# Performance work log

Measured on AMD Instinct MI355X. Metric: run time of the kernel, lower is better.

Reference implementation:

```python
import jax, jax.numpy as jnp
import numpy as np

B, X, C = 8, 256, 256  # batch, feature axis, topfreq

def setup_inputs() -> dict:
    key = jax.random.key(0)
    k1, k2, k3, k4 = jax.random.split(key, 4)
    return {
        "amplitude": jax.random.normal(k1, (B, X, C), dtype=jnp.float32),
        "phase": jax.random.normal(k2, (B, X, C), dtype=jnp.float32),
        "A": jax.random.normal(k3, (C, C), dtype=jnp.float32),
        "w_amplitude": jnp.asarray(0.5, dtype=jnp.float32),
        "w_phase": jnp.asarray(0.5, dtype=jnp.float32),
        # uniform noise for gumbel sampling; keep away from 0 to avoid -log(-log(0))
        "gumbel_u": jax.random.uniform(k4, (B, C, C, 2), dtype=jnp.float32, minval=1e-6, maxval=1.0),
    }

def reference(amplitude, phase, A, w_amplitude, w_phase, gumbel_u):
    # pairwise diffs: (b, x, c, c)
    a_diff = amplitude[..., :, None] - amplitude[..., None, :]
    p_diff = phase[..., :, None] - phase[..., None, :]
    fused = w_amplitude * a_diff + w_phase * p_diff
    # einsum 'dd,bxcd->bxcd' == multiply by diag(A) along last dim
    temp = jnp.diagonal(A) * fused
    # einsum 'bxcd,bxcd->bcd' == sum of squares over x
    dist = jnp.sum(temp * temp, axis=1)  # (b, c, c)
    exp_dist = 1.0 / (dist + 1e-10)
    eye = jnp.eye(C, dtype=exp_dist.dtype)
    off_diag = 1.0 - eye
    exp_dist = exp_dist * off_diag
    exp_max = jax.lax.stop_gradient(jnp.max(exp_dist, axis=-1, keepdims=True))
    p = exp_dist / exp_max
    p = (p * off_diag + eye) * 0.99  # (b, c, c) in (0, 0.99]
    # bernoulli via 2-class gumbel-softmax (tau=1, hard, straight-through)
    logit = jnp.log(p / (1.0 - p))
    logits = jnp.stack([logit, -logit], axis=-1)  # (b, c, c, 2)
    g = -jnp.log(-jnp.log(gumbel_u))
    y = jax.nn.softmax(logits + g, axis=-1)
    y0 = y[..., 0]
    hard0 = (y0 > y[..., 1]).astype(y.dtype)
    sample = hard0 - jax.lax.stop_gradient(y0) + y0  # straight-through
    mask = sample.mean(axis=0)  # (c, c)
    return mask
```

## Files before the change

### kernel.cpp

```cpp
#include <hip/hip_runtime.h>

#define BB 8
#define XX 256
#define CC 256
#define TCD 8
#define TCE 4
#define G  8
#define SPLIT 4
#define XH (XX / SPLIT)



__device__ __forceinline__ void epilogue(
    float dist0, float dist1, float dist2, float dist3,
    int b, int c0, int d, const float* __restrict__ gu,
    float* __restrict__ out, float (*wmax)[4])
{
    float ed[TCE];
    ed[0] = (d == c0)     ? 0.0f : __fdiv_rn(1.0f, __fadd_rn(dist0, 1e-10f));
    ed[1] = (d == c0 + 1) ? 0.0f : __fdiv_rn(1.0f, __fadd_rn(dist1, 1e-10f));
    ed[2] = (d == c0 + 2) ? 0.0f : __fdiv_rn(1.0f, __fadd_rn(dist2, 1e-10f));
    ed[3] = (d == c0 + 3) ? 0.0f : __fdiv_rn(1.0f, __fadd_rn(dist3, 1e-10f));

    const int wave = threadIdx.x >> 6;
    const int lane = threadIdx.x & 63;
#pragma unroll
    for (int j = 0; j < TCE; ++j) {
        float v = ed[j];
#pragma unroll
        for (int m = 1; m < 64; m <<= 1) v = fmaxf(v, __shfl_xor(v, m));
        if (lane == 0) wmax[j][wave] = v;
    }
    __syncthreads();

#pragma unroll
    for (int j = 0; j < TCE; ++j) {
        const int c = c0 + j;
        float em = fmaxf(fmaxf(wmax[j][0], wmax[j][1]), fmaxf(wmax[j][2], wmax[j][3]));
        float p;
        if (d == c) {
            p = 0.99f;
        } else {
            p = __fmul_rn(__fdiv_rn(ed[j], em), 0.99f);
        }
        float logit = logf(__fdiv_rn(p, __fsub_rn(1.0f, p)));

        const float2 g2 = *(const float2*)(gu + (((size_t)b * CC + c) * CC + d) * 2);
        float g0 = -logf(-logf(g2.x));
        float g1 = -logf(-logf(g2.y));

        float a0 = __fadd_rn(logit, g0);
        float a1 = __fadd_rn(-logit, g1);
        float m  = fmaxf(a0, a1);
        float e0 = expf(__fsub_rn(a0, m));
        float e1 = expf(__fsub_rn(a1, m));
        float s  = __fadd_rn(e0, e1);
        float y0 = __fdiv_rn(e0, s);
        float y1 = __fdiv_rn(e1, s);
        if (y0 > y1) {
            atomicAdd(&out[(size_t)c * CC + d], 0.125f);
        }
    }
}


__global__ __launch_bounds__(256) void k_u(
    const float* __restrict__ amp, const float* __restrict__ ph,
    const float* __restrict__ wAp, const float* __restrict__ wPp,
    float* __restrict__ u, float* __restrict__ out)
{
    const float wa = wAp[0], wp = wPp[0];
    const int i = blockIdx.x * 256 + threadIdx.x;
    const float4 a = ((const float4*)amp)[i];
    const float4 p = ((const float4*)ph)[i];
    float4 r;
    r.x = __fadd_rn(__fmul_rn(wa, a.x), __fmul_rn(wp, p.x));
    r.y = __fadd_rn(__fmul_rn(wa, a.y), __fmul_rn(wp, p.y));
    r.z = __fadd_rn(__fmul_rn(wa, a.z), __fmul_rn(wp, p.z));
    r.w = __fadd_rn(__fmul_rn(wa, a.w), __fmul_rn(wp, p.w));
    ((float4*)u)[i] = r;

    if (blockIdx.x < 64) {
        ((float4*)out)[blockIdx.x * 256 + threadIdx.x] = make_float4(0.f, 0.f, 0.f, 0.f);
    }
}

#define ULOAD(BU, GIDX) {                                  \
    const float* _p = ud_ptr + (size_t)(GIDX) * G * CC;    \
    _Pragma("unroll")                                      \
    for (int i = 0; i < G; ++i) BU[i] = _p[(size_t)i * CC]; }

#define UCOMP(BU, GIDX) {                                  \
    const int _xb = (GIDX) * G;                            \
    _Pragma("unroll")                                      \
    for (int i = 0; i < G; ++i) {                          \
        const float udv = BU[i];                           \
        const float4 cA = colsU[_xb + i][0];               \
        const float4 cB = colsU[_xb + i][1];               \
        gacc0 = fmaf(cA.x, udv, gacc0);                    \
        gacc1 = fmaf(cA.y, udv, gacc1);                    \
        gacc2 = fmaf(cA.z, udv, gacc2);                    \
        gacc3 = fmaf(cA.w, udv, gacc3);                    \
        gacc4 = fmaf(cB.x, udv, gacc4);                    \
        gacc5 = fmaf(cB.y, udv, gacc5);                    \
        gacc6 = fmaf(cB.z, udv, gacc6);                    \
        gacc7 = fmaf(cB.w, udv, gacc7);                    \
        sacc  = fmaf(udv, udv, sacc);                      \
    } }

__global__ __launch_bounds__(256, 4) void k_dist(
    const float* __restrict__ u,
    float* __restrict__ wsd)
{
    const int d    = threadIdx.x;
    const int c0   = blockIdx.x * TCD;
    const int b    = blockIdx.y;
    const int x0   = blockIdx.z * XH;

    __shared__ float4 colsU[XH][2];
    if (threadIdx.x < 2 * XH) {
        const int x = threadIdx.x >> 1;
        const int h = threadIdx.x & 1;
        colsU[x][h] =
            *(const float4*)(u + ((size_t)b * XX + x0 + x) * CC + c0 + 4 * h);
    }
    __syncthreads();

    const float* ud_ptr = u + ((size_t)b * XX + x0) * CC + d;

    float gacc0 = 0.f, gacc1 = 0.f, gacc2 = 0.f, gacc3 = 0.f;
    float gacc4 = 0.f, gacc5 = 0.f, gacc6 = 0.f, gacc7 = 0.f, sacc = 0.f;

    constexpr int NGH = XH / G;
    float b0[G], b1[G];
    ULOAD(b0, 0)
    for (int g = 0; g + 2 < NGH; g += 2) {
        ULOAD(b1, g + 1)
        UCOMP(b0, g)
        ULOAD(b0, g + 2)
        UCOMP(b1, g + 1)
    }
    ULOAD(b1, NGH - 1)
    UCOMP(b0, NGH - 2)
    UCOMP(b1, NGH - 1)

    __shared__ float sS[CC];
    sS[d] = sacc;
    __syncthreads();

    float* w = wsd + (((size_t)blockIdx.z * BB + b) * CC + c0) * CC + d;
    w[0 * CC] = fmaf(-2.0f, gacc0, __fadd_rn(sS[c0 + 0], sacc));
    w[1 * CC] = fmaf(-2.0f, gacc1, __fadd_rn(sS[c0 + 1], sacc));
    w[2 * CC] = fmaf(-2.0f, gacc2, __fadd_rn(sS[c0 + 2], sacc));
    w[3 * CC] = fmaf(-2.0f, gacc3, __fadd_rn(sS[c0 + 3], sacc));
    w[4 * CC] = fmaf(-2.0f, gacc4, __fadd_rn(sS[c0 + 4], sacc));
    w[5 * CC] = fmaf(-2.0f, gacc5, __fadd_rn(sS[c0 + 5], sacc));
    w[6 * CC] = fmaf(-2.0f, gacc6, __fadd_rn(sS[c0 + 6], sacc));
    w[7 * CC] = fmaf(-2.0f, gacc7, __fadd_rn(sS[c0 + 7], sacc));
}

__global__ __launch_bounds__(256, 4) void k_epi(
    const float* __restrict__ wsd, const float* __restrict__ A,
    const float* __restrict__ gu,  float* __restrict__ out)
{
    const int d  = threadIdx.x;
    const int c0 = blockIdx.x * TCE;
    const int b  = blockIdx.y;

    const float dAd  = A[(size_t)d * CC + d];
    const float dAd2 = __fmul_rn(dAd, dAd);

    float dist[TCE];
#pragma unroll
    for (int j = 0; j < TCE; ++j) {
        const size_t ro = ((size_t)b * CC + c0 + j) * CC + d;
        float p = wsd[ro];
#pragma unroll
        for (int h = 1; h < SPLIT; ++h)
            p = __fadd_rn(p, wsd[(size_t)h * BB * CC * CC + ro]);
        dist[j] = __fmul_rn(dAd2, p);
    }

    __shared__ float wmax[TCE][4];
    epilogue(dist[0], dist[1], dist[2], dist[3], b, c0, d, gu, out, wmax);
}


#define STEPU(UC, ACC) {                         \
    float diff = __fsub_rn(UC, ud);              \
    float t    = __fmul_rn(dAd, diff);           \
    float sq   = __fmul_rn(t, t);                \
    ACC = __fadd_rn(ACC, sq);                    \
}

#define LOADG(BA, BP, GIDX) {                    \
    const float* _a = ampbd + (size_t)(GIDX) * G * CC; \
    const float* _p = phbd  + (size_t)(GIDX) * G * CC; \
    _Pragma("unroll")                            \
    for (int i = 0; i < G; ++i) {                \
        BA[i] = _a[(size_t)i * CC];              \
        BP[i] = _p[(size_t)i * CC];              \
    }                                            \
}

#define COMPG(BA, BP, GIDX) {                    \
    const int _xb = (GIDX) * G;                  \
    _Pragma("unroll")                            \
    for (int i = 0; i < G; ++i) {                \
        const float av = BA[i];                  \
        const float pv = BP[i];                  \
        const float ud = __fadd_rn(__fmul_rn(wa, av), __fmul_rn(wp, pv)); \
        const float4 uc = cols[_xb + i];         \
        STEPU(uc.x, acc0)                        \
        STEPU(uc.y, acc1)                        \
        STEPU(uc.z, acc2)                        \
        STEPU(uc.w, acc3)                        \
    }                                            \
}

__global__ __launch_bounds__(256, 2) void k_fused(
    const float* __restrict__ amp, const float* __restrict__ ph,
    const float* __restrict__ A,   const float* __restrict__ wAp,
    const float* __restrict__ wPp, const float* __restrict__ gu,
    float* __restrict__ out)
{
    const int d  = threadIdx.x;
    const int c0 = blockIdx.x * TCE;
    const int b  = blockIdx.y;

    const float wa = wAp[0];
    const float wp = wPp[0];

    __shared__ float4 cols[XX];
    {
        const int x = threadIdx.x;
        const size_t base = ((size_t)b * XX + x) * CC + c0;
        const float4 a4 = *(const float4*)(amp + base);
        const float4 p4 = *(const float4*)(ph  + base);
        float4 uu;
        uu.x = __fadd_rn(__fmul_rn(wa, a4.x), __fmul_rn(wp, p4.x));
        uu.y = __fadd_rn(__fmul_rn(wa, a4.y), __fmul_rn(wp, p4.y));
        uu.z = __fadd_rn(__fmul_rn(wa, a4.z), __fmul_rn(wp, p4.z));
        uu.w = __fadd_rn(__fmul_rn(wa, a4.w), __fmul_rn(wp, p4.w));
        cols[x] = uu;
    }
    __syncthreads();

    const float dAd = A[(size_t)d * CC + d];
    const float* ampbd = amp + (size_t)b * XX * CC + d;
    const float* phbd  = ph  + (size_t)b * XX * CC + d;

    float acc0 = 0.0f, acc1 = 0.0f, acc2 = 0.0f, acc3 = 0.0f;
    constexpr int NG = XX / G;
    {
        float b0A[G], b0P[G], b1A[G], b1P[G];
        LOADG(b0A, b0P, 0)
        for (int g = 0; g + 2 < NG; g += 2) {
            LOADG(b1A, b1P, g + 1)
            COMPG(b0A, b0P, g)
            LOADG(b0A, b0P, g + 2)
            COMPG(b1A, b1P, g + 1)
        }
        LOADG(b1A, b1P, NG - 1)
        COMPG(b0A, b0P, NG - 2)
        COMPG(b1A, b1P, NG - 1)
    }

    __shared__ float wmax[TCE][4];
    epilogue(acc0, acc1, acc2, acc3, b, c0, d, gu, out, wmax);
}

extern "C" void kernel_launch(void* const* d_in, const int* in_sizes, int n_in,
                              void* d_out, int out_size, void* d_ws, size_t ws_size,
                              hipStream_t stream) {
    const float* amp = (const float*)d_in[0];
    const float* ph  = (const float*)d_in[1];
    const float* A   = (const float*)d_in[2];
    const float* wa  = (const float*)d_in[3];
    const float* wp  = (const float*)d_in[4];
    const float* gu  = (const float*)d_in[5];
    float* out = (float*)d_out;

    const size_t uElems = (size_t)BB * XX * CC;
    const size_t pElems = (size_t)SPLIT * BB * CC * CC;
    const size_t need = (uElems + pElems) * sizeof(float);
    if (ws_size >= need) {
        float* ud  = (float*)d_ws;
        float* wsd = ud + uElems;
        k_u<<<uElems / 4 / 256, 256, 0, stream>>>(amp, ph, wa, wp, ud, out);
        dim3 g1(CC / TCD, BB, SPLIT);
        k_dist<<<g1, 256, 0, stream>>>(ud, wsd);
        dim3 g2(CC / TCE, BB);
        k_epi<<<g2, 256, 0, stream>>>(wsd, A, gu, out);
    } else {
        hipMemsetAsync(out, 0, (size_t)CC * CC * sizeof(float), stream);
        dim3 g(CC / TCE, BB);
        k_fused<<<g, 256, 0, stream>>>(amp, ph, A, wa, wp, gu, out);
    }
}
```

Before: 83.42 us.

## Fuse split-X distance and epilogue kernels into one 1024-thread block

Merges the split-X distance kernel and the epilogue kernel into a single kernel with 1024 threads per block, where four thread groups each handle a quarter of the X axis and reduce their partials through shared memory instead of a global workspace. This removes one kernel launch and the round trip of 4*B*C*C partial sums through global memory. In exchange the grid shrinks to 256 blocks of 1024 threads, each block needing about 45 KB of shared memory, which may limit occupancy and per-CU parallelism.

```diff
diff --git a/kernel.cpp b/kernel.cpp
--- a/kernel.cpp
+++ b/kernel.cpp
@@ -6,62 +6,9 @@
 #define TCD 8
 #define TCE 4
 #define G  8
-#define SPLIT 4
-#define XH (XX / SPLIT)
-
-
-
-__device__ __forceinline__ void epilogue(
-    float dist0, float dist1, float dist2, float dist3,
-    int b, int c0, int d, const float* __restrict__ gu,
-    float* __restrict__ out, float (*wmax)[4])
-{
-    float ed[TCE];
-    ed[0] = (d == c0)     ? 0.0f : __fdiv_rn(1.0f, __fadd_rn(dist0, 1e-10f));
-    ed[1] = (d == c0 + 1) ? 0.0f : __fdiv_rn(1.0f, __fadd_rn(dist1, 1e-10f));
-    ed[2] = (d == c0 + 2) ? 0.0f : __fdiv_rn(1.0f, __fadd_rn(dist2, 1e-10f));
-    ed[3] = (d == c0 + 3) ? 0.0f : __fdiv_rn(1.0f, __fadd_rn(dist3, 1e-10f));
-
-    const int wave = threadIdx.x >> 6;
-    const int lane = threadIdx.x & 63;
-#pragma unroll
-    for (int j = 0; j < TCE; ++j) {
-        float v = ed[j];
-#pragma unroll
-        for (int m = 1; m < 64; m <<= 1) v = fmaxf(v, __shfl_xor(v, m));
-        if (lane == 0) wmax[j][wave] = v;
-    }
-    __syncthreads();
-
-#pragma unroll
-    for (int j = 0; j < TCE; ++j) {
-        const int c = c0 + j;
-        float em = fmaxf(fmaxf(wmax[j][0], wmax[j][1]), fmaxf(wmax[j][2], wmax[j][3]));
-        float p;
-        if (d == c) {
-            p = 0.99f;
-        } else {
-            p = __fmul_rn(__fdiv_rn(ed[j], em), 0.99f);
-        }
-        float logit = logf(__fdiv_rn(p, __fsub_rn(1.0f, p)));
-
-        const float2 g2 = *(const float2*)(gu + (((size_t)b * CC + c) * CC + d) * 2);
-        float g0 = -logf(-logf(g2.x));
-        float g1 = -logf(-logf(g2.y));
-
-        float a0 = __fadd_rn(logit, g0);
-        float a1 = __fadd_rn(-logit, g1);
-        float m  = fmaxf(a0, a1);
-        float e0 = expf(__fsub_rn(a0, m));
-        float e1 = expf(__fsub_rn(a1, m));
-        float s  = __fadd_rn(e0, e1);
-        float y0 = __fdiv_rn(e0, s);
-        float y1 = __fdiv_rn(e1, s);
-        if (y0 > y1) {
-            atomicAdd(&out[(size_t)c * CC + d], 0.125f);
-        }
-    }
-}
+#define NCH 4
+#define XH (XX / NCH)
+
 
 
 __global__ __launch_bounds__(256) void k_u(
@@ -91,7 +38,7 @@
     for (int i = 0; i < G; ++i) BU[i] = _p[(size_t)i * CC]; }
 
 #define UCOMP(BU, GIDX) {                                  \
-    const int _xb = (GIDX) * G;                            \
+    const int _xb = x0 + (GIDX) * G;                       \
     _Pragma("unroll")                                      \
     for (int i = 0; i < G; ++i) {                          \
         const float udv = BU[i];                           \
@@ -108,83 +55,176 @@
         sacc  = fmaf(udv, udv, sacc);                      \
     } }
 
-__global__ __launch_bounds__(256, 4) void k_dist(
+__global__ __launch_bounds__(1024, 4) void k_main(
     const float* __restrict__ u,
-    float* __restrict__ wsd)
+    const float* __restrict__ A,
+    const float* __restrict__ gu,
+    float* __restrict__ out)
 {
-    const int d    = threadIdx.x;
-    const int c0   = blockIdx.x * TCD;
-    const int b    = blockIdx.y;
-    const int x0   = blockIdx.z * XH;
-
-    __shared__ float4 colsU[XH][2];
-    if (threadIdx.x < 2 * XH) {
-        const int x = threadIdx.x >> 1;
-        const int h = threadIdx.x & 1;
-        colsU[x][h] =
-            *(const float4*)(u + ((size_t)b * XX + x0 + x) * CC + c0 + 4 * h);
-    }
-    __syncthreads();
+    const int tid = threadIdx.x;
+    const int c0  = blockIdx.x * TCD;
+    const int b   = blockIdx.y;
+
+    __shared__ float4 colsU[XX][2];
+    __shared__ float  sS[NCH][CC];
+    __shared__ float  pw[NCH][CC][9];
+    __shared__ float  wmax[TCD][4];
+
+    if (tid < 512) {
+        const int x = tid >> 1, h = tid & 1;
+        colsU[x][h] = *(const float4*)(u + ((size_t)b * XX + x) * CC + c0 + 4 * h);
+    }
+    __syncthreads();
+
+    const int d     = tid & 255;
+    const int chunk = tid >> 8;
+    const int x0    = chunk * XH;
 
     const float* ud_ptr = u + ((size_t)b * XX + x0) * CC + d;
 
-    float gacc0 = 0.f, gacc1 = 0.f, gacc2 = 0.f, gacc3 = 0.f;
-    float gacc4 = 0.f, gacc5 = 0.f, gacc6 = 0.f, gacc7 = 0.f, sacc = 0.f;
+    float gacc0=0.f, gacc1=0.f, gacc2=0.f, gacc3=0.f;
+    float gacc4=0.f, gacc5=0.f, gacc6=0.f, gacc7=0.f, sacc=0.f;
 
     constexpr int NGH = XH / G;
-    float b0[G], b1[G];
-    ULOAD(b0, 0)
-    for (int g = 0; g + 2 < NGH; g += 2) {
-        ULOAD(b1, g + 1)
-        UCOMP(b0, g)
-        ULOAD(b0, g + 2)
-        UCOMP(b1, g + 1)
-    }
-    ULOAD(b1, NGH - 1)
-    UCOMP(b0, NGH - 2)
-    UCOMP(b1, NGH - 1)
-
-    __shared__ float sS[CC];
-    sS[d] = sacc;
-    __syncthreads();
-
-    float* w = wsd + (((size_t)blockIdx.z * BB + b) * CC + c0) * CC + d;
-    w[0 * CC] = fmaf(-2.0f, gacc0, __fadd_rn(sS[c0 + 0], sacc));
-    w[1 * CC] = fmaf(-2.0f, gacc1, __fadd_rn(sS[c0 + 1], sacc));
-    w[2 * CC] = fmaf(-2.0f, gacc2, __fadd_rn(sS[c0 + 2], sacc));
-    w[3 * CC] = fmaf(-2.0f, gacc3, __fadd_rn(sS[c0 + 3], sacc));
-    w[4 * CC] = fmaf(-2.0f, gacc4, __fadd_rn(sS[c0 + 4], sacc));
-    w[5 * CC] = fmaf(-2.0f, gacc5, __fadd_rn(sS[c0 + 5], sacc));
-    w[6 * CC] = fmaf(-2.0f, gacc6, __fadd_rn(sS[c0 + 6], sacc));
-    w[7 * CC] = fmaf(-2.0f, gacc7, __fadd_rn(sS[c0 + 7], sacc));
-}
-
-__global__ __launch_bounds__(256, 4) void k_epi(
-    const float* __restrict__ wsd, const float* __restrict__ A,
-    const float* __restrict__ gu,  float* __restrict__ out)
+    {
+        float b0[G], b1[G];
+        ULOAD(b0, 0)
+        for (int g = 0; g + 2 < NGH; g += 2) {
+            ULOAD(b1, g + 1)
+            UCOMP(b0, g)
+            ULOAD(b0, g + 2)
+            UCOMP(b1, g + 1)
+        }
+        ULOAD(b1, NGH - 1)
+        UCOMP(b0, NGH - 2)
+        UCOMP(b1, NGH - 1)
+    }
+
+    sS[chunk][d] = sacc;
+    __syncthreads();
+
+    pw[chunk][d][0] = fmaf(-2.0f, gacc0, __fadd_rn(sS[chunk][c0 + 0], sacc));
+    pw[chunk][d][1] = fmaf(-2.0f, gacc1, __fadd_rn(sS[chunk][c0 + 1], sacc));
+    pw[chunk][d][2] = fmaf(-2.0f, gacc2, __fadd_rn(sS[chunk][c0 + 2], sacc));
+    pw[chunk][d][3] = fmaf(-2.0f, gacc3, __fadd_rn(sS[chunk][c0 + 3], sacc));
+    pw[chunk][d][4] = fmaf(-2.0f, gacc4, __fadd_rn(sS[chunk][c0 + 4], sacc));
+    pw[chunk][d][5] = fmaf(-2.0f, gacc5, __fadd_rn(sS[chunk][c0 + 5], sacc));
+    pw[chunk][d][6] = fmaf(-2.0f, gacc6, __fadd_rn(sS[chunk][c0 + 6], sacc));
+    pw[chunk][d][7] = fmaf(-2.0f, gacc7, __fadd_rn(sS[chunk][c0 + 7], sacc));
+    __syncthreads();
+
+    const int de   = tid & 255;
+    const int j2   = tid >> 8;
+    const int wv   = (tid >> 6) & 3;
+    const int lane = tid & 63;
+
+    const float dAd  = A[(size_t)de * CC + de];
+    const float dAd2 = __fmul_rn(dAd, dAd);
+
+    float edv[2];
+#pragma unroll
+    for (int k = 0; k < 2; ++k) {
+        const int j = 2 * j2 + k;
+        float p = pw[0][de][j];
+        p = __fadd_rn(p, pw[1][de][j]);
+        p = __fadd_rn(p, pw[2][de][j]);
+        p = __fadd_rn(p, pw[3][de][j]);
+        const float dist = __fmul_rn(dAd2, p);
+        edv[k] = (de == c0 + j) ? 0.0f : __fdiv_rn(1.0f, __fadd_rn(dist, 1e-10f));
+    }
+
+#pragma unroll
+    for (int k = 0; k < 2; ++k) {
+        float v = edv[k];
+#pragma unroll
+        for (int m = 1; m < 64; m <<= 1) v = fmaxf(v, __shfl_xor(v, m));
+        if (lane == 0) wmax[2 * j2 + k][wv] = v;
+    }
+    __syncthreads();
+
+#pragma unroll
+    for (int k = 0; k < 2; ++k) {
+        const int j = 2 * j2 + k;
+        const int c = c0 + j;
+        float em = fmaxf(fmaxf(wmax[j][0], wmax[j][1]), fmaxf(wmax[j][2], wmax[j][3]));
+        float p;
+        if (de == c) {
+            p = 0.99f;
+        } else {
+            p = __fmul_rn(__fdiv_rn(edv[k], em), 0.99f);
+        }
+        float logit = logf(__fdiv_rn(p, __fsub_rn(1.0f, p)));
+
+        const float2 g2 = *(const float2*)(gu + (((size_t)b * CC + c) * CC + de) * 2);
+        float g0 = -logf(-logf(g2.x));
+        float g1 = -logf(-logf(g2.y));
+
+        float a0 = __fadd_rn(logit, g0);
+        float a1 = __fadd_rn(-logit, g1);
+        float m  = fmaxf(a0, a1);
+        float e0 = expf(__fsub_rn(a0, m));
+        float e1 = expf(__fsub_rn(a1, m));
+        float s  = __fadd_rn(e0, e1);
+        float y0 = __fdiv_rn(e0, s);
+        float y1 = __fdiv_rn(e1, s);
+        if (y0 > y1) {
+            atomicAdd(&out[(size_t)c * CC + de], 0.125f);
+        }
+    }
+}
+
+
+__device__ __forceinline__ void epilogue4(
+    float dist0, float dist1, float dist2, float dist3,
+    int b, int c0, int d, const float* __restrict__ gu,
+    float* __restrict__ out, float (*wmax)[4])
 {
-    const int d  = threadIdx.x;
-    const int c0 = blockIdx.x * TCE;
-    const int b  = blockIdx.y;
-
-    const float dAd  = A[(size_t)d * CC + d];
-    const float dAd2 = __fmul_rn(dAd, dAd);
-
-    float dist[TCE];
+    float ed[TCE];
+    ed[0] = (d == c0)     ? 0.0f : __fdiv_rn(1.0f, __fadd_rn(dist0, 1e-10f));
+    ed[1] = (d == c0 + 1) ? 0.0f : __fdiv_rn(1.0f, __fadd_rn(dist1, 1e-10f));
+    ed[2] = (d == c0 + 2) ? 0.0f : __fdiv_rn(1.0f, __fadd_rn(dist2, 1e-10f));
+    ed[3] = (d == c0 + 3) ? 0.0f : __fdiv_rn(1.0f, __fadd_rn(dist3, 1e-10f));
+
+    const int wave = threadIdx.x >> 6;
+    const int lane = threadIdx.x & 63;
 #pragma unroll
     for (int j = 0; j < TCE; ++j) {
-        const size_t ro = ((size_t)b * CC + c0 + j) * CC + d;
-        float p = wsd[ro];
-#pragma unroll
-        for (int h = 1; h < SPLIT; ++h)
-            p = __fadd_rn(p, wsd[(size_t)h * BB * CC * CC + ro]);
-        dist[j] = __fmul_rn(dAd2, p);
-    }
-
-    __shared__ float wmax[TCE][4];
-    epilogue(dist[0], dist[1], dist[2], dist[3], b, c0, d, gu, out, wmax);
-}
-
+        float v = ed[j];
+#pragma unroll
+        for (int m = 1; m < 64; m <<= 1) v = fmaxf(v, __shfl_xor(v, m));
+        if (lane == 0) wmax[j][wave] = v;
+    }
+    __syncthreads();
+
+#pragma unroll
+    for (int j = 0; j < TCE; ++j) {
+        const int c = c0 + j;
+        float em = fmaxf(fmaxf(wmax[j][0], wmax[j][1]), fmaxf(wmax[j][2], wmax[j][3]));
+        float p;
+        if (d == c) {
+            p = 0.99f;
+        } else {
+            p = __fmul_rn(__fdiv_rn(ed[j], em), 0.99f);
+        }
+        float logit = logf(__fdiv_rn(p, __fsub_rn(1.0f, p)));
+
+        const float2 g2 = *(const float2*)(gu + (((size_t)b * CC + c) * CC + d) * 2);
+        float g0 = -logf(-logf(g2.x));
+        float g1 = -logf(-logf(g2.y));
+
+        float a0 = __fadd_rn(logit, g0);
+        float a1 = __fadd_rn(-logit, g1);
+        float m  = fmaxf(a0, a1);
+        float e0 = expf(__fsub_rn(a0, m));
+        float e1 = expf(__fsub_rn(a1, m));
+        float s  = __fadd_rn(e0, e1);
+        float y0 = __fdiv_rn(e0, s);
+        float y1 = __fdiv_rn(e1, s);
+        if (y0 > y1) {
+            atomicAdd(&out[(size_t)c * CC + d], 0.125f);
+        }
+    }
+}
 
 #define STEPU(UC, ACC) {                         \
     float diff = __fsub_rn(UC, ud);              \
@@ -267,7 +307,7 @@
     }
 
     __shared__ float wmax[TCE][4];
-    epilogue(acc0, acc1, acc2, acc3, b, c0, d, gu, out, wmax);
+    epilogue4(acc0, acc1, acc2, acc3, b, c0, d, gu, out, wmax);
 }
 
 extern "C" void kernel_launch(void* const* d_in, const int* in_sizes, int n_in,
@@ -282,16 +322,12 @@
     float* out = (float*)d_out;
 
     const size_t uElems = (size_t)BB * XX * CC;
-    const size_t pElems = (size_t)SPLIT * BB * CC * CC;
-    const size_t need = (uElems + pElems) * sizeof(float);
+    const size_t need = uElems * sizeof(float);
     if (ws_size >= need) {
-        float* ud  = (float*)d_ws;
-        float* wsd = ud + uElems;
+        float* ud = (float*)d_ws;
         k_u<<<uElems / 4 / 256, 256, 0, stream>>>(amp, ph, wa, wp, ud, out);
-        dim3 g1(CC / TCD, BB, SPLIT);
-        k_dist<<<g1, 256, 0, stream>>>(ud, wsd);
-        dim3 g2(CC / TCE, BB);
-        k_epi<<<g2, 256, 0, stream>>>(wsd, A, gu, out);
+        dim3 g(CC / TCD, BB);
+        k_main<<<g, 1024, 0, stream>>>(ud, A, gu, out);
     } else {
         hipMemsetAsync(out, 0, (size_t)CC * CC * sizeof(float), stream);
         dim3 g(CC / TCE, BB);
```

Measured after the change: 94.83 us. 13.7% more time.
